# Optimization experiments

Hardware: AMD Instinct MI355X
Metric: run time of the kernel (lower is better)

## Reference

```python
import jax, jax.numpy as jnp
import numpy as np

KERNEL_MUL = 2.0
KERNEL_NUM = 5
STRUCT_W = 0.1

N_NODES = 4096
D_FEAT = 128
N_EDGES = 65536


def setup_inputs() -> dict:
    key = jax.random.key(0)
    k1, k2, k3, k4 = jax.random.split(key, 4)
    return {
        "source_features": jax.random.normal(k1, (N_NODES, D_FEAT), jnp.float32),
        "target_features": jax.random.normal(k2, (N_NODES, D_FEAT), jnp.float32),
        "source_edge_index": jax.random.randint(k3, (2, N_EDGES), 0, N_NODES, jnp.int32),
        "target_edge_index": jax.random.randint(k4, (2, N_EDGES), 0, N_NODES, jnp.int32),
    }


def _augment(feats, edge_index):
    # feats: [n, d]; edge_index: [2, E]
    n = feats.shape[0]
    # in-degree (torch_geometric degree on edge_index[1]), normalized by n-1
    deg = jnp.zeros(n, feats.dtype).at[edge_index[1]].add(1.0)
    norm_deg = deg / (n - 1)
    # dense adjacency (to_dense_adj sums duplicate edges)
    A = jnp.zeros((n, n), feats.dtype).at[edge_index[0], edge_index[1]].add(1.0)
    M = (A > 0).astype(feats.dtype)  # binary neighbor mask (nonzero rows)
    d = M.sum(axis=1)  # number of neighbors per node
    # triangles[v] = sum_{i,j in N(v)} A[i,j] / 2  == ((M @ A) * M).sum(1) / 2
    tri = ((M @ A) * M).sum(axis=1) / 2.0
    max_edges = d * (d - 1) / 2.0
    clustering = jnp.where(d >= 2.0, tri / jnp.maximum(max_edges, 1.0), 0.0)
    struct = jnp.stack([norm_deg, jnp.log1p(clustering)], axis=1)  # [n, 2]
    return jnp.concatenate([feats, STRUCT_W * struct], axis=1)


def _rbf_mmd(X, Y):
    nx, ny = X.shape[0], Y.shape[0]
    XY = jnp.concatenate([X, Y], axis=0)  # [N, d+2]
    sq = jnp.sum(XY * XY, axis=1)
    # squared euclidean distances (cdist ** 2), clamped for numerical safety
    dists = jnp.maximum(sq[:, None] + sq[None, :] - 2.0 * (XY @ XY.T), 0.0)
    N = nx + ny
    # adaptive bandwidth: median of strictly-upper-triangle distances
    triu_mask = jnp.triu(jnp.ones((N, N), bool), k=1)
    sigma = jnp.nanmedian(jnp.where(triu_mask, dists, jnp.nan))
    K = jnp.zeros_like(dists)
    for i in range(KERNEL_NUM):  # fixed small multiscale loop
        bw = sigma * (KERNEL_MUL ** (i - KERNEL_NUM // 2))
        K = K + jnp.exp(-dists / (2.0 * bw))
    K = K / KERNEL_NUM
    K_XX, K_YY, K_XY = K[:nx, :nx], K[nx:, nx:], K[:nx, nx:]
    mxx = (K_XX.sum() - jnp.trace(K_XX)) / (nx * (nx - 1))
    myy = (K_YY.sum() - jnp.trace(K_YY)) / (ny * (ny - 1))
    mxy = K_XY.mean()
    return jnp.maximum(mxx + myy - 2.0 * mxy, 0.0)


def reference(source_features, target_features, source_edge_index, target_edge_index):
    X = _augment(source_features, source_edge_index)
    Y = _augment(target_features, target_edge_index)
    return _rbf_mmd(X, Y)
```

## Files before the change

### kernel.cpp

```cpp
#include <hip/hip_runtime.h>
#include <math.h>

#define NN    4096
#define DF    128
#define NE    65536
#define NTOT  8192
#define DP    132
#define TILE  128
#define KC    44
#define NTILE 64
#define NBLK  2080
#define R0    16775167u
#define R1    16775168u
#define FINF  __int_as_float(0x7f800000)

#define OFF_MB   0ULL
#define OFF_H1   4194304ULL
#define OFF_HMID 4210688ULL
#define OFF_HLOW 4218880ULL
#define OFF_DEG  4227072ULL
#define OFF_TRI  4259840ULL
#define ZERO_BYTES 4292608ULL
#define OFF_XY   4292608ULL
#define OFF_SQ   8617984ULL
#define OFF_BS   8650752ULL
#define OFF_SEL  8667392ULL
#define OFF_SIG  8667456ULL
#define OFF_D    8667520ULL
#define DBYTES   136314880ULL
#define WS_CACHED (OFF_D + DBYTES)


__global__ __launch_bounds__(256) void build_k(const int* __restrict__ eiS, const int* __restrict__ eiT,
                                               unsigned* __restrict__ Mb, int* __restrict__ degc){
  int gid = blockIdx.x*256 + threadIdx.x;
  int g = gid >> 16, e = gid & 65535;
  const int* ei = g ? eiT : eiS;
  unsigned* M = Mb + (size_t)g*NN*128;
  int* dg = degc + g*NN;
  int s = ei[e], t = ei[NE + e];
  atomicOr(&M[(size_t)s*128 + (t>>5)], 1u << (t&31));
  atomicAdd(&dg[t], 1);
}

#define GPB 16
__global__ __launch_bounds__(256) void tri_k(const int* __restrict__ eiS, const int* __restrict__ eiT,
                                             const unsigned* __restrict__ Mb, int* __restrict__ tric){
  int g  = blockIdx.x >> 8;
  int nb = blockIdx.x & 255;
  const int* ei = g ? eiT : eiS;
  const unsigned* M = Mb + (size_t)g*NN*128;
  int* tr = tric + g*NN;
  __shared__ unsigned lm[128*20];
  __shared__ int lcnt[GPB];
  int tid = threadIdx.x;
  for(int idx=tid; idx<128*GPB; idx+=256){
    int w = idx & 127, gg = idx >> 7;
    lm[w*20+gg] = M[(size_t)(nb*GPB+gg)*128 + w];
  }
  if(tid < GPB) lcnt[tid]=0;
  __syncthreads();
  int cnt[GPB];
  #pragma unroll
  for(int q=0;q<GPB;++q) cnt[q]=0;
  for(int e=tid; e<NE; e+=256){
    int s = ei[e], t = ei[NE+e];
    int ws_ = s>>5, bs = s&31, wt = t>>5, bt = t&31;
    const uint4* ps4 = (const uint4*)&lm[ws_*20];
    const uint4* pt4 = (const uint4*)&lm[wt*20];
    unsigned a_[GPB], b_[GPB];
    ((uint4*)a_)[0]=ps4[0]; ((uint4*)a_)[1]=ps4[1]; ((uint4*)a_)[2]=ps4[2]; ((uint4*)a_)[3]=ps4[3];
    ((uint4*)b_)[0]=pt4[0]; ((uint4*)b_)[1]=pt4[1]; ((uint4*)b_)[2]=pt4[2]; ((uint4*)b_)[3]=pt4[3];
    #pragma unroll
    for(int q=0;q<GPB;++q) cnt[q] += (int)((a_[q]>>bs) & (b_[q]>>bt) & 1u);
  }
  #pragma unroll
  for(int q=0;q<GPB;++q){
    int v = cnt[q];
    for(int off=32; off; off>>=1) v += __shfl_down(v, off);
    if((tid&63)==0) atomicAdd(&lcnt[q], v);
  }
  __syncthreads();
  if(tid < GPB) tr[nb*GPB + tid] = lcnt[tid];
}

__global__ __launch_bounds__(64) void finalize_k(const float* __restrict__ featS, const float* __restrict__ featT,
                                                 const unsigned* __restrict__ Mb, const int* __restrict__ degc,
                                                 const int* __restrict__ tric, float* __restrict__ XY,
                                                 float* __restrict__ sq){
  int b = blockIdx.x;
  int g = b >> 12, i = b & 4095;
  int lane = threadIdx.x;
  const unsigned* Mr = Mb + (size_t)g*NN*128 + (size_t)i*128;
  int pc = __popc(Mr[lane]) + __popc(Mr[64+lane]);
  for(int off=32; off; off>>=1) pc += __shfl_down(pc, off);
  pc = __shfl(pc, 0);
  const float* feats = g ? featT : featS;
  float* row = XY + (size_t)(g*NN + i)*DP;
  float v0 = feats[(size_t)i*DF + lane];
  float v1 = feats[(size_t)i*DF + 64 + lane];
  row[lane] = v0; row[64+lane] = v1;
  float s0 = v0*v0 + v1*v1;
  if(lane==0){
    float degf = (float)degc[g*NN+i];
    float nd   = degf / 4095.0f;
    float dd   = (float)pc;
    float tri  = 0.5f * (float)tric[g*NN+i];
    float me   = dd*(dd-1.0f)*0.5f;
    float cl   = (dd >= 2.0f) ? (tri / fmaxf(me, 1.0f)) : 0.0f;
    float f0 = 0.1f * nd;
    float f1 = 0.1f * log1pf(cl);
    row[128]=f0; row[129]=f1; row[130]=0.0f; row[131]=0.0f;
    s0 += f0*f0 + f1*f1;
  }
  for(int off=32; off; off>>=1) s0 += __shfl_down(s0, off);
  if(lane==0) sq[g*NN+i] = s0;
}

template<int MODE>
__global__ __launch_bounds__(256) void pair_k(const float* __restrict__ XY, const float* __restrict__ sq,
                                              unsigned* __restrict__ hist1, unsigned* __restrict__ hmid,
                                              unsigned* __restrict__ hlow, const unsigned* __restrict__ sel,
                                              const float* __restrict__ sigp, double* __restrict__ blockSums,
                                              float* __restrict__ Dout){
  int t = blockIdx.x, bi = 0;
  while(t >= NTILE - bi){ t -= NTILE - bi; ++bi; }
  int bj = bi + t;
  __shared__ float As[KC][TILE];
  __shared__ float Bs[KC][TILE];
  int tid = threadIdx.x;
  int trw = tid >> 4, tcl = tid & 15;
  float acc[8][8];
  #pragma unroll
  for(int r=0;r<8;++r){
    #pragma unroll
    for(int c=0;c<8;++c) acc[r][c]=0.f;
  }
  int i0 = bi*TILE, j0 = bj*TILE;
  for(int kc=0; kc<3; ++kc){
    for(int idx=tid; idx<TILE*11; idx+=256){
      int r = idx/11, q = idx - r*11;
      float4 va = *(const float4*)&XY[(size_t)(i0+r)*DP + kc*KC + q*4];
      float4 vb = *(const float4*)&XY[(size_t)(j0+r)*DP + kc*KC + q*4];
      int k = q*4;
      As[k][r]=va.x; As[k+1][r]=va.y; As[k+2][r]=va.z; As[k+3][r]=va.w;
      Bs[k][r]=vb.x; Bs[k+1][r]=vb.y; Bs[k+2][r]=vb.z; Bs[k+3][r]=vb.w;
    }
    __syncthreads();
    #pragma unroll 4
    for(int k=0;k<KC;++k){
      float a[8], b[8];
      *(float4*)&a[0] = *(const float4*)&As[k][trw*8];
      *(float4*)&a[4] = *(const float4*)&As[k][trw*8+4];
      *(float4*)&b[0] = *(const float4*)&Bs[k][tcl*8];
      *(float4*)&b[4] = *(const float4*)&Bs[k][tcl*8+4];
      #pragma unroll
      for(int r=0;r<8;++r){
        #pragma unroll
        for(int c=0;c<8;++c) acc[r][c] = fmaf(a[r], b[c], acc[r][c]);
      }
    }
    __syncthreads();
  }
  float sqi[8], sqj[8];
  #pragma unroll
  for(int r=0;r<8;++r) sqi[r] = sq[i0 + trw*8 + r];
  #pragma unroll
  for(int c=0;c<8;++c) sqj[c] = sq[j0 + tcl*8 + c];

  if constexpr (MODE==0 || MODE==3){
    __shared__ unsigned lh[4096];
    for(int x=tid;x<4096;x+=256) lh[x]=0u;
    __syncthreads();
    #pragma unroll
    for(int r=0;r<8;++r){
      float rowd[8];
      #pragma unroll
      for(int c=0;c<8;++c){
        int i = i0 + trw*8 + r, j = j0 + tcl*8 + c;
        bool valid = (bi!=bj) || (i<j);
        float d = fmaxf(sqi[r]+sqj[c]-2.0f*acc[r][c], 0.0f);
        rowd[c] = valid ? d : FINF;
        if(valid) atomicAdd(&lh[__float_as_uint(d)>>20], 1u);
      }
      if constexpr (MODE==3){
        float* rp = Dout + (size_t)blockIdx.x*16384 + (size_t)(trw*8+r)*128 + tcl*8;
        *(float4*)rp       = make_float4(rowd[0],rowd[1],rowd[2],rowd[3]);
        *(float4*)(rp+4)   = make_float4(rowd[4],rowd[5],rowd[6],rowd[7]);
      }
    }
    __syncthreads();
    for(int x=tid;x<4096;x+=256){ unsigned v=lh[x]; if(v) atomicAdd(&hist1[x], v); }
  } else if constexpr (MODE==4 || MODE==5){
    __shared__ unsigned lh2[2048];
    for(int x=tid;x<2048;x+=256) lh2[x]=0u;
    __syncthreads();
    unsigned m0, m1;
    if constexpr (MODE==4){ m0=sel[0]; m1=sel[1]; }
    else                  { m0=(sel[0]<<10)|sel[4]; m1=(sel[1]<<10)|sel[5]; }
    #pragma unroll
    for(int r=0;r<8;++r){
      #pragma unroll
      for(int c=0;c<8;++c){
        int i = i0 + trw*8 + r, j = j0 + tcl*8 + c;
        if(bi!=bj || i<j){
          float d = fmaxf(sqi[r]+sqj[c]-2.0f*acc[r][c], 0.0f);
          unsigned bits = __float_as_uint(d);
          unsigned key = (MODE==4) ? (bits>>20) : (bits>>10);
          unsigned bin = (MODE==4) ? ((bits>>10)&1023u) : (bits&1023u);
          if(key==m0)      atomicAdd(&lh2[bin], 1u);
          else if(key==m1) atomicAdd(&lh2[1024+bin], 1u);
        }
      }
    }
    __syncthreads();
    unsigned* hout = (MODE==4) ? hmid : hlow;
    for(int x=tid;x<2048;x+=256){ unsigned v=lh2[x]; if(v) atomicAdd(&hout[x], v); }
  } else {
    float sig = *sigp;
    float inv = 1.0f/sig;
    float k0=2.0f*inv, k1=inv, k2=0.5f*inv, k3=0.25f*inv, k4=0.125f*inv;
    double lsum = 0.0;
    #pragma unroll
    for(int r=0;r<8;++r){
      #pragma unroll
      for(int c=0;c<8;++c){
        int i = i0 + trw*8 + r, j = j0 + tcl*8 + c;
        if(bi!=bj || i<j){
          float d = fmaxf(sqi[r]+sqj[c]-2.0f*acc[r][c], 0.0f);
          float kv = expf(-d*k0)+expf(-d*k1)+expf(-d*k2)+expf(-d*k3)+expf(-d*k4);
          lsum += (double)kv;
        }
      }
    }
    for(int off=32; off; off>>=1) lsum += __shfl_down(lsum, off);
    __shared__ double redbuf[4];
    if((tid&63)==0) redbuf[tid>>6] = lsum;
    __syncthreads();
    if(tid==0) blockSums[blockIdx.x] = (redbuf[0]+redbuf[1]+redbuf[2]+redbuf[3])*0.2;
  }
}

template<int LVL>
__global__ __launch_bounds__(256) void hist_stream_k(const float* __restrict__ D, const unsigned* __restrict__ sel,
                                                     unsigned* __restrict__ hout){
  __shared__ unsigned lh[2048];
  int tid = threadIdx.x;
  for(int x=tid;x<2048;x+=256) lh[x]=0u;
  __syncthreads();
  unsigned m0, m1;
  if constexpr (LVL==0){ m0=sel[0]; m1=sel[1]; }
  else                 { m0=(sel[0]<<10)|sel[4]; m1=(sel[1]<<10)|sel[5]; }
  const float4* P = (const float4*)(D + (size_t)blockIdx.x*16384);
  #pragma unroll
  for(int k=0;k<16;++k){
    float4 v = P[tid + k*256];
    float vals[4] = {v.x, v.y, v.z, v.w};
    #pragma unroll
    for(int q=0;q<4;++q){
      unsigned bits = __float_as_uint(vals[q]);
      unsigned key = (LVL==0) ? (bits>>20) : (bits>>10);
      unsigned bin = (LVL==0) ? ((bits>>10)&1023u) : (bits&1023u);
      if(key==m0)      atomicAdd(&lh[bin], 1u);
      else if(key==m1) atomicAdd(&lh[1024+bin], 1u);
    }
  }
  __syncthreads();
  for(int x=tid;x<2048;x+=256){ unsigned v=lh[x]; if(v) atomicAdd(&hout[x], v); }
}

__global__ __launch_bounds__(256) void ksum_k(const float* __restrict__ D, const float* __restrict__ sigp,
                                              double* __restrict__ blockSums){
  float sig = *sigp;
  float inv = 1.0f/sig;
  float k0=2.0f*inv, k1=inv, k2=0.5f*inv, k3=0.25f*inv, k4=0.125f*inv;
  const float4* P = (const float4*)(D + (size_t)blockIdx.x*16384);
  int tid = threadIdx.x;
  double lsum = 0.0;
  #pragma unroll
  for(int k=0;k<16;++k){
    float4 v = P[tid + k*256];
    float vals[4] = {v.x, v.y, v.z, v.w};
    #pragma unroll
    for(int q=0;q<4;++q){
      float d = vals[q];
      float kv = expf(-d*k0)+expf(-d*k1)+expf(-d*k2)+expf(-d*k3)+expf(-d*k4);
      lsum += (double)kv;
    }
  }
  for(int off=32; off; off>>=1) lsum += __shfl_down(lsum, off);
  __shared__ double redbuf[4];
  if((tid&63)==0) redbuf[tid>>6] = lsum;
  __syncthreads();
  if(tid==0) blockSums[blockIdx.x] = (redbuf[0]+redbuf[1]+redbuf[2]+redbuf[3])*0.2;
}

__global__ __launch_bounds__(256) void sel1_k(const unsigned* __restrict__ hist1, unsigned* __restrict__ sel){
  __shared__ unsigned part[256];
  int tid = threadIdx.x;
  unsigned s = 0;
  #pragma unroll
  for(int k=0;k<16;++k) s += hist1[tid*16+k];
  part[tid] = s;
  __syncthreads();
  if(tid==0){
    const unsigned ranks[2] = {R0, R1};
    unsigned segs[2], bases[2];
    unsigned cum = 0; int found = 0;
    for(int i=0; i<256 && found<2; ++i){
      unsigned nx = cum + part[i];
      while(found<2 && ranks[found] < nx){ segs[found]=i; bases[found]=cum; ++found; }
      cum = nx;
    }
    for(int tg=0; tg<2; ++tg){
      unsigned c2 = bases[tg];
      for(int b=segs[tg]*16;; ++b){
        unsigned nx = c2 + hist1[b];
        if(ranks[tg] < nx){ sel[tg]=(unsigned)b; sel[2+tg]=ranks[tg]-c2; break; }
        c2 = nx;
      }
    }
  }
}

__global__ __launch_bounds__(1024) void selB_k(const unsigned* __restrict__ hmid, unsigned* __restrict__ sel){
  __shared__ unsigned buf[1024];
  __shared__ unsigned res[4];
  int tid = threadIdx.x;
  for(int tgt=0; tgt<2; ++tgt){
    bool useA = (tgt==0) || (sel[1]==sel[0]);
    const unsigned* H = hmid + (useA ? 0 : 1024);
    unsigned rank = sel[2+tgt];
    buf[tid] = H[tid];
    __syncthreads();
    for(int off=1; off<1024; off<<=1){
      unsigned v = buf[tid];
      unsigned a = (tid>=off) ? buf[tid-off] : 0u;
      __syncthreads();
      buf[tid] = v + a;
      __syncthreads();
    }
    unsigned prev = tid ? buf[tid-1] : 0u;
    if(rank < buf[tid] && rank >= prev){ res[2*tgt]=(unsigned)tid; res[2*tgt+1]=rank-prev; }
    __syncthreads();
  }
  if(tid==0){ sel[4]=res[0]; sel[6]=res[1]; sel[5]=res[2]; sel[7]=res[3]; }
}

__global__ __launch_bounds__(1024) void selC_k(const unsigned* __restrict__ hlow, const unsigned* __restrict__ sel,
                                               float* __restrict__ sigp){
  __shared__ unsigned buf[1024];
  __shared__ unsigned outbits[2];
  int tid = threadIdx.x;
  for(int tgt=0; tgt<2; ++tgt){
    bool useA = (tgt==0) || ((sel[1]==sel[0]) && (sel[5]==sel[4]));
    const unsigned* H = hlow + (useA ? 0 : 1024);
    unsigned rank = sel[6+tgt];
    buf[tid] = H[tid];
    __syncthreads();
    for(int off=1; off<1024; off<<=1){
      unsigned v = buf[tid];
      unsigned a = (tid>=off) ? buf[tid-off] : 0u;
      __syncthreads();
      buf[tid] = v + a;
      __syncthreads();
    }
    unsigned prev = tid ? buf[tid-1] : 0u;
    if(rank < buf[tid] && rank >= prev){
      outbits[tgt] = (sel[tgt]<<20) | (sel[4+tgt]<<10) | (unsigned)tid;
    }
    __syncthreads();
  }
  if(tid==0){
    float v0 = __uint_as_float(outbits[0]);
    float v1 = __uint_as_float(outbits[1]);
    *sigp = 0.5f*(v0+v1);
  }
}

__global__ __launch_bounds__(256) void final_k(const double* __restrict__ blockSums, float* __restrict__ out){
  __shared__ double cls[3][256];
  int tid = threadIdx.x;
  double l0=0, l1=0, l2=0;
  for(int b=tid; b<NBLK; b+=256){
    int t=b, bi=0;
    while(t >= NTILE - bi){ t -= NTILE - bi; ++bi; }
    int bj = bi + t;
    double v = blockSums[b];
    if(bj < 32) l0 += v;
    else if(bi >= 32) l2 += v;
    else l1 += v;
  }
  cls[0][tid]=l0; cls[1][tid]=l1; cls[2][tid]=l2;
  __syncthreads();
  for(int off=128; off; off>>=1){
    if(tid<off){ cls[0][tid]+=cls[0][tid+off]; cls[1][tid]+=cls[1][tid+off]; cls[2][tid]+=cls[2][tid+off]; }
    __syncthreads();
  }
  if(tid==0){
    double sxx=cls[0][0], sxy=cls[1][0], syy=cls[2][0];
    double mxx = (2.0*sxx)/((double)NN*(NN-1));
    double myy = (2.0*syy)/((double)NN*(NN-1));
    double mxy = sxy/((double)NN*(double)NN);
    double r = mxx + myy - 2.0*mxy;
    out[0] = fmaxf((float)r, 0.0f);
  }
}

extern "C" void kernel_launch(void* const* d_in, const int* in_sizes, int n_in,
                              void* d_out, int out_size, void* d_ws, size_t ws_size,
                              hipStream_t stream){
  (void)in_sizes; (void)n_in; (void)out_size;
  const float* featS = (const float*)d_in[0];
  const float* featT = (const float*)d_in[1];
  const int*   eiS   = (const int*)d_in[2];
  const int*   eiT   = (const int*)d_in[3];
  char* ws = (char*)d_ws;
  unsigned* Mb    = (unsigned*)(ws + OFF_MB);
  unsigned* hist1 = (unsigned*)(ws + OFF_H1);
  unsigned* hmid  = (unsigned*)(ws + OFF_HMID);
  unsigned* hlow  = (unsigned*)(ws + OFF_HLOW);
  int*      degc  = (int*)(ws + OFF_DEG);
  int*      tric  = (int*)(ws + OFF_TRI);
  float*    XY    = (float*)(ws + OFF_XY);
  float*    sq    = (float*)(ws + OFF_SQ);
  double*   bsums = (double*)(ws + OFF_BS);
  unsigned* sel   = (unsigned*)(ws + OFF_SEL);
  float*    sigp  = (float*)(ws + OFF_SIG);
  float*    Dbuf  = (float*)(ws + OFF_D);
  float*    out   = (float*)d_out;

  const bool cached = (ws_size >= WS_CACHED);

  hipMemsetAsync(ws, 0, (size_t)ZERO_BYTES, stream);

  build_k   <<<512, 256, 0, stream>>>(eiS, eiT, Mb, degc);
  tri_k     <<<512, 256, 0, stream>>>(eiS, eiT, Mb, tric);
  finalize_k<<<NTOT, 64, 0, stream>>>(featS, featT, Mb, degc, tric, XY, sq);

  if(cached){
    pair_k<3>       <<<NBLK, 256, 0, stream>>>(XY, sq, hist1, hmid, hlow, sel, sigp, bsums, Dbuf);
    sel1_k          <<<1, 256, 0, stream>>>(hist1, sel);
    hist_stream_k<0><<<NBLK, 256, 0, stream>>>(Dbuf, sel, hmid);
    selB_k          <<<1, 1024, 0, stream>>>(hmid, sel);
    hist_stream_k<1><<<NBLK, 256, 0, stream>>>(Dbuf, sel, hlow);
    selC_k          <<<1, 1024, 0, stream>>>(hlow, sel, sigp);
    ksum_k          <<<NBLK, 256, 0, stream>>>(Dbuf, sigp, bsums);
  } else {
    pair_k<0>       <<<NBLK, 256, 0, stream>>>(XY, sq, hist1, hmid, hlow, sel, sigp, bsums, Dbuf);
    sel1_k          <<<1, 256, 0, stream>>>(hist1, sel);
    pair_k<4>       <<<NBLK, 256, 0, stream>>>(XY, sq, hist1, hmid, hlow, sel, sigp, bsums, Dbuf);
    selB_k          <<<1, 1024, 0, stream>>>(hmid, sel);
    pair_k<5>       <<<NBLK, 256, 0, stream>>>(XY, sq, hist1, hmid, hlow, sel, sigp, bsums, Dbuf);
    selC_k          <<<1, 1024, 0, stream>>>(hlow, sel, sigp);
    pair_k<2>       <<<NBLK, 256, 0, stream>>>(XY, sq, hist1, hmid, hlow, sel, sigp, bsums, Dbuf);
  }

  final_k  <<<1, 256, 0, stream>>>(bsums, out);
}
```

Measured before the change: 565.3 us.

## Store augmented features transposed and share one LDS buffer across phases

The augmented feature matrix is now written feature-major (132 x 8192), so the GEMM tile loader reads contiguous float4 columns and stores them straight into shared memory with no scatter-transpose. The separate A/B tiles, histogram and reduction shared arrays are merged into one aliased buffer, which reduces LDS footprint and may allow higher occupancy. The cost is that finalize_k now writes strided, uncoalesced column stores.

```diff
diff --git a/kernel.cpp b/kernel.cpp
--- a/kernel.cpp
+++ b/kernel.cpp
@@ -5,7 +5,6 @@
 #define DF    128
 #define NE    65536
 #define NTOT  8192
-#define DP    132
 #define TILE  128
 #define KC    44
 #define NTILE 64
@@ -21,7 +20,7 @@
 #define OFF_DEG  4227072ULL
 #define OFF_TRI  4259840ULL
 #define ZERO_BYTES 4292608ULL
-#define OFF_XY   4292608ULL
+#define OFF_XYT  4292608ULL
 #define OFF_SQ   8617984ULL
 #define OFF_BS   8650752ULL
 #define OFF_SEL  8667392ULL
@@ -86,7 +85,7 @@
 
 __global__ __launch_bounds__(64) void finalize_k(const float* __restrict__ featS, const float* __restrict__ featT,
                                                  const unsigned* __restrict__ Mb, const int* __restrict__ degc,
-                                                 const int* __restrict__ tric, float* __restrict__ XY,
+                                                 const int* __restrict__ tric, float* __restrict__ XYT,
                                                  float* __restrict__ sq){
   int b = blockIdx.x;
   int g = b >> 12, i = b & 4095;
@@ -96,10 +95,11 @@
   for(int off=32; off; off>>=1) pc += __shfl_down(pc, off);
   pc = __shfl(pc, 0);
   const float* feats = g ? featT : featS;
-  float* row = XY + (size_t)(g*NN + i)*DP;
+  int n = g*NN + i;
   float v0 = feats[(size_t)i*DF + lane];
   float v1 = feats[(size_t)i*DF + 64 + lane];
-  row[lane] = v0; row[64+lane] = v1;
+  XYT[(size_t)lane*NTOT + n]      = v0;
+  XYT[(size_t)(64+lane)*NTOT + n] = v1;
   float s0 = v0*v0 + v1*v1;
   if(lane==0){
     float degf = (float)degc[g*NN+i];
@@ -110,7 +110,10 @@
     float cl   = (dd >= 2.0f) ? (tri / fmaxf(me, 1.0f)) : 0.0f;
     float f0 = 0.1f * nd;
     float f1 = 0.1f * log1pf(cl);
-    row[128]=f0; row[129]=f1; row[130]=0.0f; row[131]=0.0f;
+    XYT[(size_t)128*NTOT + n] = f0;
+    XYT[(size_t)129*NTOT + n] = f1;
+    XYT[(size_t)130*NTOT + n] = 0.0f;
+    XYT[(size_t)131*NTOT + n] = 0.0f;
     s0 += f0*f0 + f1*f1;
   }
   for(int off=32; off; off>>=1) s0 += __shfl_down(s0, off);
@@ -118,7 +121,7 @@
 }
 
 template<int MODE>
-__global__ __launch_bounds__(256) void pair_k(const float* __restrict__ XY, const float* __restrict__ sq,
+__global__ __launch_bounds__(256) void pair_k(const float* __restrict__ XYT, const float* __restrict__ sq,
                                               unsigned* __restrict__ hist1, unsigned* __restrict__ hmid,
                                               unsigned* __restrict__ hlow, const unsigned* __restrict__ sel,
                                               const float* __restrict__ sigp, double* __restrict__ blockSums,
@@ -126,8 +129,9 @@
   int t = blockIdx.x, bi = 0;
   while(t >= NTILE - bi){ t -= NTILE - bi; ++bi; }
   int bj = bi + t;
-  __shared__ float As[KC][TILE];
-  __shared__ float Bs[KC][TILE];
+  __shared__ float4 smem4[2816];
+  float* As = (float*)smem4;
+  float* Bs = As + KC*TILE;
   int tid = threadIdx.x;
   int trw = tid >> 4, tcl = tid & 15;
   float acc[8][8];
@@ -138,22 +142,25 @@
   }
   int i0 = bi*TILE, j0 = bj*TILE;
   for(int kc=0; kc<3; ++kc){
-    for(int idx=tid; idx<TILE*11; idx+=256){
-      int r = idx/11, q = idx - r*11;
-      float4 va = *(const float4*)&XY[(size_t)(i0+r)*DP + kc*KC + q*4];
-      float4 vb = *(const float4*)&XY[(size_t)(j0+r)*DP + kc*KC + q*4];
-      int k = q*4;
-      As[k][r]=va.x; As[k+1][r]=va.y; As[k+2][r]=va.z; As[k+3][r]=va.w;
-      Bs[k][r]=vb.x; Bs[k+1][r]=vb.y; Bs[k+2][r]=vb.z; Bs[k+3][r]=vb.w;
+    #pragma unroll
+    for(int s=0;s<11;++s){
+      int idx = tid + s*256;
+      int isB = idx >= 1408;
+      int l = isB ? (idx-1408) : idx;
+      int k = l >> 5, c4 = l & 31;
+      int col = (isB ? j0 : i0) + c4*4;
+      smem4[idx] = *(const float4*)&XYT[(size_t)(kc*KC+k)*NTOT + col];
     }
     __syncthreads();
     #pragma unroll 4
     for(int k=0;k<KC;++k){
       float a[8], b[8];
-      *(float4*)&a[0] = *(const float4*)&As[k][trw*8];
-      *(float4*)&a[4] = *(const float4*)&As[k][trw*8+4];
-      *(float4*)&b[0] = *(const float4*)&Bs[k][tcl*8];
-      *(float4*)&b[4] = *(const float4*)&Bs[k][tcl*8+4];
+      const float* Ak = As + k*TILE;
+      const float* Bk = Bs + k*TILE;
+      *(float4*)&a[0] = *(const float4*)&Ak[trw*8];
+      *(float4*)&a[4] = *(const float4*)&Ak[trw*8+4];
+      *(float4*)&b[0] = *(const float4*)&Bk[tcl*8];
+      *(float4*)&b[4] = *(const float4*)&Bk[tcl*8+4];
       #pragma unroll
       for(int r=0;r<8;++r){
         #pragma unroll
@@ -169,7 +176,7 @@
   for(int c=0;c<8;++c) sqj[c] = sq[j0 + tcl*8 + c];
 
   if constexpr (MODE==0 || MODE==3){
-    __shared__ unsigned lh[4096];
+    unsigned* lh = (unsigned*)smem4;
     for(int x=tid;x<4096;x+=256) lh[x]=0u;
     __syncthreads();
     #pragma unroll
@@ -192,7 +199,7 @@
     __syncthreads();
     for(int x=tid;x<4096;x+=256){ unsigned v=lh[x]; if(v) atomicAdd(&hist1[x], v); }
   } else if constexpr (MODE==4 || MODE==5){
-    __shared__ unsigned lh2[2048];
+    unsigned* lh2 = (unsigned*)smem4;
     for(int x=tid;x<2048;x+=256) lh2[x]=0u;
     __syncthreads();
     unsigned m0, m1;
@@ -234,7 +241,7 @@
       }
     }
     for(int off=32; off; off>>=1) lsum += __shfl_down(lsum, off);
-    __shared__ double redbuf[4];
+    double* redbuf = (double*)smem4;
     if((tid&63)==0) redbuf[tid>>6] = lsum;
     __syncthreads();
     if(tid==0) blockSums[blockIdx.x] = (redbuf[0]+redbuf[1]+redbuf[2]+redbuf[3])*0.2;
@@ -422,7 +429,7 @@
   unsigned* hlow  = (unsigned*)(ws + OFF_HLOW);
   int*      degc  = (int*)(ws + OFF_DEG);
   int*      tric  = (int*)(ws + OFF_TRI);
-  float*    XY    = (float*)(ws + OFF_XY);
+  float*    XYT   = (float*)(ws + OFF_XYT);
   float*    sq    = (float*)(ws + OFF_SQ);
   double*   bsums = (double*)(ws + OFF_BS);
   unsigned* sel   = (unsigned*)(ws + OFF_SEL);
@@ -436,10 +443,10 @@
 
   build_k   <<<512, 256, 0, stream>>>(eiS, eiT, Mb, degc);
   tri_k     <<<512, 256, 0, stream>>>(eiS, eiT, Mb, tric);
-  finalize_k<<<NTOT, 64, 0, stream>>>(featS, featT, Mb, degc, tric, XY, sq);
+  finalize_k<<<NTOT, 64, 0, stream>>>(featS, featT, Mb, degc, tric, XYT, sq);
 
   if(cached){
-    pair_k<3>       <<<NBLK, 256, 0, stream>>>(XY, sq, hist1, hmid, hlow, sel, sigp, bsums, Dbuf);
+    pair_k<3>       <<<NBLK, 256, 0, stream>>>(XYT, sq, hist1, hmid, hlow, sel, sigp, bsums, Dbuf);
     sel1_k          <<<1, 256, 0, stream>>>(hist1, sel);
     hist_stream_k<0><<<NBLK, 256, 0, stream>>>(Dbuf, sel, hmid);
     selB_k          <<<1, 1024, 0, stream>>>(hmid, sel);
@@ -447,13 +454,13 @@
     selC_k          <<<1, 1024, 0, stream>>>(hlow, sel, sigp);
     ksum_k          <<<NBLK, 256, 0, stream>>>(Dbuf, sigp, bsums);
   } else {
-    pair_k<0>       <<<NBLK, 256, 0, stream>>>(XY, sq, hist1, hmid, hlow, sel, sigp, bsums, Dbuf);
+    pair_k<0>       <<<NBLK, 256, 0, stream>>>(XYT, sq, hist1, hmid, hlow, sel, sigp, bsums, Dbuf);
     sel1_k          <<<1, 256, 0, stream>>>(hist1, sel);
-    pair_k<4>       <<<NBLK, 256, 0, stream>>>(XY, sq, hist1, hmid, hlow, sel, sigp, bsums, Dbuf);
+    pair_k<4>       <<<NBLK, 256, 0, stream>>>(XYT, sq, hist1, hmid, hlow, sel, sigp, bsums, Dbuf);
     selB_k          <<<1, 1024, 0, stream>>>(hmid, sel);
-    pair_k<5>       <<<NBLK, 256, 0, stream>>>(XY, sq, hist1, hmid, hlow, sel, sigp, bsums, Dbuf);
+    pair_k<5>       <<<NBLK, 256, 0, stream>>>(XYT, sq, hist1, hmid, hlow, sel, sigp, bsums, Dbuf);
     selC_k          <<<1, 1024, 0, stream>>>(hlow, sel, sigp);
-    pair_k<2>       <<<NBLK, 256, 0, stream>>>(XY, sq, hist1, hmid, hlow, sel, sigp, bsums, Dbuf);
+    pair_k<2>       <<<NBLK, 256, 0, stream>>>(XYT, sq, hist1, hmid, hlow, sel, sigp, bsums, Dbuf);
   }
 
   final_k  <<<1, 256, 0, stream>>>(bsums, out);
```

After: 541.1 us. 1.04x faster.
